# Kernel optimization log

Hardware: AMD Instinct MI355X
Metric: run time of the kernel (lower is better)

## Reference

```python
import math
import jax, jax.numpy as jnp
import numpy as np

L = 4        # n_layer
H = 8        # n_head
C = 512      # n_embd
V = 50257    # vocab_size
BLK = 1024   # block_size
R = 8        # lora_rank
LORA_SCALING = 32.0 / 8.0  # lora_alpha / lora_rank
B, T = 2, 1024


def _layernorm(x, g, b, eps=1e-5):
    m = jnp.mean(x, axis=-1, keepdims=True)
    v = jnp.var(x, axis=-1, keepdims=True)
    return (x - m) / jnp.sqrt(v + eps) * g + b


def _new_gelu(x):
    # 0.5*x*(1+tanh(sqrt(2/pi)*(x+0.044715*x^3)))
    return 0.5 * x * (1.0 + jnp.tanh(math.sqrt(2.0 / math.pi) * (x + 0.044715 * x ** 3)))


def _lora_linear(x, W, A, Bm):
    # nn.Linear (no bias) + LoRA low-rank update (dropout is identity in eval)
    return x @ W.T + LORA_SCALING * ((x @ A.T) @ Bm.T)


def setup_inputs() -> dict:
    key = jax.random.key(0)
    ks = jax.random.split(key, 16)
    s = 0.02  # GPT-2 init std
    inp = {
        'idx': jax.random.randint(ks[0], (B, T), 0, V, dtype=jnp.int64),
        'wte': jax.random.normal(ks[1], (V, C), jnp.float32) * s,
        'wpe': jax.random.normal(ks[2], (BLK, C), jnp.float32) * s,
        'ln1_g': jnp.ones((L, C), jnp.float32),
        'ln1_b': jnp.zeros((L, C), jnp.float32),
        'attn_w': jax.random.normal(ks[3], (L, 3 * C, C), jnp.float32) * s,
        'attn_lA': jax.random.normal(ks[4], (L, R, C), jnp.float32) * s,
        'attn_lB': jax.random.normal(ks[5], (L, 3 * C, R), jnp.float32) * s,
        'proj_w': jax.random.normal(ks[6], (L, C, C), jnp.float32) * (s / math.sqrt(2 * L)),
        'proj_lA': jax.random.normal(ks[7], (L, R, C), jnp.float32) * s,
        'proj_lB': jax.random.normal(ks[8], (L, C, R), jnp.float32) * s,
        'ln2_g': jnp.ones((L, C), jnp.float32),
        'ln2_b': jnp.zeros((L, C), jnp.float32),
        'fc_w': jax.random.normal(ks[9], (L, 4 * C, C), jnp.float32) * s,
        'fc_b': jnp.zeros((L, 4 * C), jnp.float32),
        'mproj_w': jax.random.normal(ks[10], (L, C, 4 * C), jnp.float32) * (s / math.sqrt(2 * L)),
        'mproj_b': jnp.zeros((L, C), jnp.float32),
        'lnf_g': jnp.ones((C,), jnp.float32),
        'lnf_b': jnp.zeros((C,), jnp.float32),
        'head_w': jax.random.normal(ks[11], (V, C), jnp.float32) * s,
    }
    return inp


def _gpt_forward(idx, wte, wpe, ln1_g, ln1_b, attn_w, attn_lA, attn_lB,
                 proj_w, proj_lA, proj_lB, ln2_g, ln2_b, fc_w, fc_b,
                 mproj_w, mproj_b, lnf_g, lnf_b, head_w):
    Bsz, Tlen = idx.shape
    hd = C // H
    x = wte[idx] + wpe[:Tlen][None, :, :]          # [B,T,C]
    mask = jnp.tril(jnp.ones((Tlen, Tlen), bool))  # causal mask
    for i in range(L):
        # --- attention ---
        h = _layernorm(x, ln1_g[i], ln1_b[i])
        qkv = _lora_linear(h, attn_w[i], attn_lA[i], attn_lB[i])  # [B,T,3C]
        q, k, v = jnp.split(qkv, 3, axis=-1)
        q = q.reshape(Bsz, Tlen, H, hd).transpose(0, 2, 1, 3)  # bhtd
        k = k.reshape(Bsz, Tlen, H, hd).transpose(0, 2, 1, 3)
        v = v.reshape(Bsz, Tlen, H, hd).transpose(0, 2, 1, 3)
        att = jnp.einsum('bhqd,bhkd->bhqk', q, k) * (1.0 / math.sqrt(hd))
        att = jnp.where(mask, att, -jnp.inf)
        att = jax.nn.softmax(att, axis=-1)
        y = jnp.einsum('bhqk,bhkd->bhqd', att, v)
        y = y.transpose(0, 2, 1, 3).reshape(Bsz, Tlen, C)
        y = _lora_linear(y, proj_w[i], proj_lA[i], proj_lB[i])
        x = x + y
        # --- MLP ---
        h2 = _layernorm(x, ln2_g[i], ln2_b[i])
        m = _new_gelu(h2 @ fc_w[i].T + fc_b[i]) @ mproj_w[i].T + mproj_b[i]
        x = x + m
    x = _layernorm(x, lnf_g, lnf_b)
    return x @ head_w.T  # logits [B,T,V]


def reference(idx, wte, wpe, ln1_g, ln1_b, attn_w, attn_lA, attn_lB,
              proj_w, proj_lA, proj_lB, ln2_g, ln2_b, fc_w, fc_b,
              mproj_w, mproj_b, lnf_g, lnf_b, head_w):
    return _gpt_forward(idx, wte, wpe, ln1_g, ln1_b, attn_w, attn_lA, attn_lB,
                        proj_w, proj_lA, proj_lB, ln2_g, ln2_b, fc_w, fc_b,
                        mproj_w, mproj_b, lnf_g, lnf_b, head_w)
```

## Files before the change

kernel.cpp:

```cpp
#include <hip/hip_runtime.h>
#include <cstdint>
#include <cstddef>

#define NLAYER 4
#define CDIM   512
#define TLEN   1024
#define BSZ    2
#define MROWS  (BSZ * TLEN)
#define VOCAB  50257
#define NHEAD  8
#define HDIM   64
#define LORA_S 4.0f

typedef unsigned short ushort_t;
typedef __attribute__((ext_vector_type(8))) short  short8;
typedef __attribute__((ext_vector_type(8))) _Float16 half8;
typedef __attribute__((ext_vector_type(4))) float  f32x4;
typedef __attribute__((ext_vector_type(4))) unsigned short us4;

__device__ inline ushort_t f2bf(float f) {
  union { float f; unsigned u; } c; c.f = f;
  unsigned u = c.u;
  u += 0x7fffu + ((u >> 16) & 1u);
  return (ushort_t)(u >> 16);
}

__device__ inline ushort_t f2h(float f) {
  union { _Float16 h; ushort_t u; } c; c.h = (_Float16)f;
  return c.u;
}

__device__ inline float gelu_f(float v) {
  float t = tanhf(0.7978845608028654f * (v + 0.044715f * v * v * v));
  return 0.5f * v * (1.0f + t);
}

__device__ inline void stage16(const ushort_t* g, ushort_t* lds) {
  __builtin_amdgcn_global_load_lds(
      (__attribute__((address_space(1))) unsigned int*)(g),
      (__attribute__((address_space(3))) unsigned int*)(lds),
      16, 0, 0);
}

template<int EPI>
__global__ __launch_bounds__(256) void gemm_bt(const ushort_t* __restrict__ A,
                                               const ushort_t* __restrict__ B,
                                               void* __restrict__ Cv,
                                               const float* __restrict__ bias,
                                               int M, int N, int K) {
  __shared__ ushort_t As[128 * 32];
  __shared__ ushort_t Bs[128 * 32];
  const int tid  = threadIdx.x;
  const int wave = tid >> 6, lane = tid & 63;
  const int m0 = blockIdx.y << 7;
  const int n0 = blockIdx.x << 7;
  const int wr = (wave >> 1) << 6;
  const int wc = (wave & 1) << 6;
  const int lr = lane & 15;
  const int kq = (lane >> 4) << 3;

  f32x4 acc[4][4];
#pragma unroll
  for (int i = 0; i < 4; ++i)
#pragma unroll
    for (int j = 0; j < 4; ++j) {
      acc[i][j][0] = 0.f; acc[i][j][1] = 0.f;
      acc[i][j][2] = 0.f; acc[i][j][3] = 0.f;
    }

  for (int k0 = 0; k0 < K; k0 += 32) {
    __syncthreads();
#pragma unroll
    for (int i = 0; i < 2; ++i) {
      int c = i * 256 + tid;
      int row = c >> 2, col = (c & 3) << 3;
      stage16(A + (size_t)(m0 + row) * K + k0 + col,
              As + ((i * 256 + (wave << 6)) << 3));
    }
#pragma unroll
    for (int i = 0; i < 2; ++i) {
      int c = i * 256 + tid;
      int row = c >> 2, col = (c & 3) << 3;
      int n = n0 + row; if (n > N - 1) n = N - 1;
      stage16(B + (size_t)n * K + k0 + col,
              Bs + ((i * 256 + (wave << 6)) << 3));
    }
    __syncthreads();

    short8 af[4], bf[4];
#pragma unroll
    for (int i = 0; i < 4; ++i)
      af[i] = *(const short8*)(As + (wr + i * 16 + lr) * 32 + kq);
#pragma unroll
    for (int j = 0; j < 4; ++j)
      bf[j] = *(const short8*)(Bs + (wc + j * 16 + lr) * 32 + kq);
#pragma unroll
    for (int i = 0; i < 4; ++i)
#pragma unroll
      for (int j = 0; j < 4; ++j)
        acc[i][j] = __builtin_amdgcn_mfma_f32_16x16x32_bf16(af[i], bf[j], acc[i][j], 0, 0, 0);
  }

  const int rq = (lane >> 4) << 2;
  const int cl = lane & 15;
#pragma unroll
  for (int i = 0; i < 4; ++i) {
    int mb = m0 + wr + i * 16 + rq;
#pragma unroll
    for (int j = 0; j < 4; ++j) {
      int col = n0 + wc + j * 16 + cl;
      if (col < N) {
        if (EPI == 0) {
          float* cp = (float*)Cv + (size_t)mb * N + col;
#pragma unroll
          for (int r = 0; r < 4; ++r) cp[(size_t)r * N] = acc[i][j][r];
        } else {
          ushort_t* cp = (ushort_t*)Cv + (size_t)mb * N + col;
          const float bb = bias[col];
#pragma unroll
          for (int r = 0; r < 4; ++r) cp[(size_t)r * N] = f2bf(gelu_f(acc[i][j][r] + bb));
        }
      }
    }
  }
}

__global__ __launch_bounds__(256) void gemm64_res(const ushort_t* __restrict__ A,
                                                  const ushort_t* __restrict__ B,
                                                  float* __restrict__ x,
                                                  const float* __restrict__ bias,
                                                  int M, int N, int K) {
  __shared__ ushort_t As[64 * 32];
  __shared__ ushort_t Bs[64 * 32];
  const int tid  = threadIdx.x;
  const int wave = tid >> 6, lane = tid & 63;
  const int m0 = blockIdx.y << 6;
  const int n0 = blockIdx.x << 6;
  const int wr = (wave >> 1) << 5;
  const int wc = (wave & 1) << 5;
  const int lr = lane & 15;
  const int kq = (lane >> 4) << 3;

  f32x4 acc[2][2];
#pragma unroll
  for (int i = 0; i < 2; ++i)
#pragma unroll
    for (int j = 0; j < 2; ++j) {
      acc[i][j][0] = 0.f; acc[i][j][1] = 0.f;
      acc[i][j][2] = 0.f; acc[i][j][3] = 0.f;
    }

  const int row = tid >> 2, col = (tid & 3) << 3;

  for (int k0 = 0; k0 < K; k0 += 32) {
    __syncthreads();
    stage16(A + (size_t)(m0 + row) * K + k0 + col, As + (wave << 9));
    stage16(B + (size_t)(n0 + row) * K + k0 + col, Bs + (wave << 9));
    __syncthreads();

    short8 af[2], bf[2];
#pragma unroll
    for (int i = 0; i < 2; ++i)
      af[i] = *(const short8*)(As + (wr + i * 16 + lr) * 32 + kq);
#pragma unroll
    for (int j = 0; j < 2; ++j)
      bf[j] = *(const short8*)(Bs + (wc + j * 16 + lr) * 32 + kq);
#pragma unroll
    for (int i = 0; i < 2; ++i)
#pragma unroll
      for (int j = 0; j < 2; ++j)
        acc[i][j] = __builtin_amdgcn_mfma_f32_16x16x32_bf16(af[i], bf[j], acc[i][j], 0, 0, 0);
  }

  const int rq = (lane >> 4) << 2;
  const int cl = lane & 15;
#pragma unroll
  for (int i = 0; i < 2; ++i) {
    int mb = m0 + wr + i * 16 + rq;
#pragma unroll
    for (int j = 0; j < 2; ++j) {
      int c = n0 + wc + j * 16 + cl;
      float bb = bias ? bias[c] : 0.f;
      float* xp = x + (size_t)mb * N + c;
#pragma unroll
      for (int r = 0; r < 4; ++r) xp[(size_t)r * N] = xp[(size_t)r * N] + acc[i][j][r] + bb;
    }
  }
}

__global__ void conv_bf16(const float* __restrict__ in, ushort_t* __restrict__ out, long n) {
  long i = ((long)blockIdx.x * 256 + threadIdx.x) * 4;
  if (i < n) {
    float4 v = *(const float4*)(in + i);
    us4 o = { f2bf(v.x), f2bf(v.y), f2bf(v.z), f2bf(v.w) };
    *(us4*)(out + i) = o;
  }
}

__global__ void conv_lora(const float* __restrict__ W, const float* __restrict__ lA,
                          const float* __restrict__ lB, ushort_t* __restrict__ out,
                          int N, long total) {
  long i = (long)blockIdx.x * 256 + threadIdx.x;
  if (i >= total) return;
  long nk = (long)N * CDIM;
  int  l  = (int)(i / nk);
  long r  = i - (long)l * nk;
  int  n  = (int)(r >> 9);
  int  k  = (int)(r & 511);
  const float* lAp = lA + (long)l * 8 * CDIM;
  const float* lBp = lB + (long)l * N * 8;
  float acc = W[i];
#pragma unroll
  for (int j = 0; j < 8; ++j) acc += LORA_S * lBp[n * 8 + j] * lAp[j * CDIM + k];
  out[i] = f2bf(acc);
}

__global__ void embed_kernel(const int* __restrict__ idx, const float* __restrict__ wte,
                             const float* __restrict__ wpe, float* __restrict__ x) {
  int i = blockIdx.x * 256 + threadIdx.x;
  int m = i >> 9, c = i & 511;
  int t = m & (TLEN - 1);
  x[i] = wte[(size_t)idx[m] * CDIM + c] + wpe[(size_t)t * CDIM + c];
}

__global__ __launch_bounds__(256) void ln_kernel(const float* __restrict__ x,
                                                 const float* __restrict__ g,
                                                 const float* __restrict__ b,
                                                 ushort_t* __restrict__ out) {
  const int m = blockIdx.x, tid = threadIdx.x;
  const float2 v = ((const float2*)(x + (size_t)m * CDIM))[tid];
  float s = v.x + v.y, ss = v.x * v.x + v.y * v.y;
#pragma unroll
  for (int off = 32; off; off >>= 1) { s += __shfl_xor(s, off); ss += __shfl_xor(ss, off); }
  __shared__ float rs[4], rss[4];
  const int w = tid >> 6, lane = tid & 63;
  if (lane == 0) { rs[w] = s; rss[w] = ss; }
  __syncthreads();
  s  = rs[0] + rs[1] + rs[2] + rs[3];
  ss = rss[0] + rss[1] + rss[2] + rss[3];
  const float mean = s * (1.f / CDIM);
  const float var  = ss * (1.f / CDIM) - mean * mean;
  const float rstd = rsqrtf(var + 1e-5f);
  const int c = tid * 2;
  out[(size_t)m * CDIM + c]     = f2bf((v.x - mean) * rstd * g[c]     + b[c]);
  out[(size_t)m * CDIM + c + 1] = f2bf((v.y - mean) * rstd * g[c + 1] + b[c + 1]);
}

__global__ __launch_bounds__(256) void attn_mfma(const float* __restrict__ qkv,
                                                 ushort_t* __restrict__ ybf) {
  __shared__ ushort_t Ks[32 * 72];
  __shared__ ushort_t Vt[64 * 40];
  __shared__ ushort_t Pl[4 * 16 * 40];

  const int tid  = threadIdx.x;
  const int wave = tid >> 6, lane = tid & 63;
  const int lr   = lane & 15;
  const int quad = lane >> 4;
  const int kq   = quad << 3;
  const int t0   = blockIdx.x << 6;
  const int bh   = blockIdx.y;
  const int bb   = bh >> 3, hh = bh & 7;
  const int qb   = t0 + (wave << 4);
  const size_t RS = 3 * CDIM;

  half8 aq[2];
  {
    const float* qr = qkv + (size_t)(bb * TLEN + qb + lr) * RS + hh * 64 + kq;
#pragma unroll
    for (int c = 0; c < 2; ++c) {
      float4 f0 = *(const float4*)(qr + c * 32);
      float4 f1 = *(const float4*)(qr + c * 32 + 4);
      half8 v;
      v[0] = (_Float16)f0.x; v[1] = (_Float16)f0.y;
      v[2] = (_Float16)f0.z; v[3] = (_Float16)f0.w;
      v[4] = (_Float16)f1.x; v[5] = (_Float16)f1.y;
      v[6] = (_Float16)f1.z; v[7] = (_Float16)f1.w;
      aq[c] = v;
    }
  }

  f32x4 o[4];
#pragma unroll
  for (int dt = 0; dt < 4; ++dt) { o[dt][0] = 0.f; o[dt][1] = 0.f; o[dt][2] = 0.f; o[dt][3] = 0.f; }
  float m[4] = { -1e30f, -1e30f, -1e30f, -1e30f };
  float l[4] = { 0.f, 0.f, 0.f, 0.f };

  const int kk    = tid & 31;
  const int dbase = (tid >> 5) << 3;

  const int ntiles = (blockIdx.x + 1) << 1;
  for (int kb = 0; kb < ntiles; ++kb) {
    const int kbase = kb << 5;
    __syncthreads();
    {
      const float* kp = qkv + (size_t)(bb * TLEN + kbase + kk) * RS + CDIM + hh * 64 + dbase;
      float4 f0 = *(const float4*)kp;
      float4 f1 = *(const float4*)(kp + 4);
      half8 kv;
      kv[0] = (_Float16)f0.x; kv[1] = (_Float16)f0.y;
      kv[2] = (_Float16)f0.z; kv[3] = (_Float16)f0.w;
      kv[4] = (_Float16)f1.x; kv[5] = (_Float16)f1.y;
      kv[6] = (_Float16)f1.z; kv[7] = (_Float16)f1.w;
      *(half8*)(Ks + kk * 72 + dbase) = kv;
      const float* vp = kp + CDIM;
      float4 g0 = *(const float4*)vp;
      float4 g1 = *(const float4*)(vp + 4);
      ushort_t vb[8] = { f2h(g0.x), f2h(g0.y), f2h(g0.z), f2h(g0.w),
                         f2h(g1.x), f2h(g1.y), f2h(g1.z), f2h(g1.w) };
#pragma unroll
      for (int j = 0; j < 8; ++j) Vt[(dbase + j) * 40 + kk] = vb[j];
    }
    __syncthreads();

    if (kbase <= qb + 15) {
      f32x4 st[2];
#pragma unroll
      for (int kt = 0; kt < 2; ++kt) {
        half8 b0 = *(const half8*)(Ks + (kt * 16 + lr) * 72 + kq);
        half8 b1 = *(const half8*)(Ks + (kt * 16 + lr) * 72 + 32 + kq);
        f32x4 acc = { 0.f, 0.f, 0.f, 0.f };
        acc = __builtin_amdgcn_mfma_f32_16x16x32_f16(aq[0], b0, acc, 0, 0, 0);
        acc = __builtin_amdgcn_mfma_f32_16x16x32_f16(aq[1], b1, acc, 0, 0, 0);
        st[kt] = acc;
      }
      float corr[4];
#pragma unroll
      for (int r = 0; r < 4; ++r) {
        const int qrow = qb + quad * 4 + r;
#pragma unroll
        for (int kt = 0; kt < 2; ++kt) {
          const int kcol = kbase + kt * 16 + lr;
          float s = st[kt][r] * 0.125f;
          st[kt][r] = (kcol <= qrow) ? s : -1e30f;
        }
        float mx = fmaxf(st[0][r], st[1][r]);
#pragma unroll
        for (int off = 8; off; off >>= 1) mx = fmaxf(mx, __shfl_xor(mx, off));
        const float mnew = fmaxf(m[r], mx);
        corr[r] = __expf(m[r] - mnew);
        m[r] = mnew;
        float p0 = __expf(st[0][r] - mnew);
        float p1 = __expf(st[1][r] - mnew);
        st[0][r] = p0; st[1][r] = p1;
        float ps = p0 + p1;
#pragma unroll
        for (int off = 8; off; off >>= 1) ps += __shfl_xor(ps, off);
        l[r] = l[r] * corr[r] + ps;
      }
#pragma unroll
      for (int dt = 0; dt < 4; ++dt)
#pragma unroll
        for (int r = 0; r < 4; ++r) o[dt][r] *= corr[r];
      ushort_t* pw = Pl + wave * 640;
#pragma unroll
      for (int kt = 0; kt < 2; ++kt)
#pragma unroll
        for (int r = 0; r < 4; ++r)
          pw[(quad * 4 + r) * 40 + kt * 16 + lr] = f2h(st[kt][r]);
      half8 ap = *(const half8*)(pw + lr * 40 + kq);
#pragma unroll
      for (int dt = 0; dt < 4; ++dt) {
        half8 bv = *(const half8*)(Vt + (dt * 16 + lr) * 40 + kq);
        o[dt] = __builtin_amdgcn_mfma_f32_16x16x32_f16(ap, bv, o[dt], 0, 0, 0);
      }
    }
  }

#pragma unroll
  for (int r = 0; r < 4; ++r) {
    const float inv = 1.0f / l[r];
    const int qrow = qb + quad * 4 + r;
    ushort_t* yp = ybf + (size_t)(bb * TLEN + qrow) * CDIM + hh * 64;
#pragma unroll
    for (int dt = 0; dt < 4; ++dt)
      yp[dt * 16 + lr] = f2bf(o[dt][r] * inv);
  }
}

extern "C" void kernel_launch(void* const* d_in, const int* in_sizes, int n_in,
                              void* d_out, int out_size, void* d_ws, size_t ws_size,
                              hipStream_t stream) {
  const int*   idx     = (const int*)  d_in[0];
  const float* wte     = (const float*)d_in[1];
  const float* wpe     = (const float*)d_in[2];
  const float* ln1_g   = (const float*)d_in[3];
  const float* ln1_b   = (const float*)d_in[4];
  const float* attn_w  = (const float*)d_in[5];
  const float* attn_lA = (const float*)d_in[6];
  const float* attn_lB = (const float*)d_in[7];
  const float* proj_w  = (const float*)d_in[8];
  const float* proj_lA = (const float*)d_in[9];
  const float* proj_lB = (const float*)d_in[10];
  const float* ln2_g   = (const float*)d_in[11];
  const float* ln2_b   = (const float*)d_in[12];
  const float* fc_w    = (const float*)d_in[13];
  const float* fc_b    = (const float*)d_in[14];
  const float* mproj_w = (const float*)d_in[15];
  const float* mproj_b = (const float*)d_in[16];
  const float* lnf_g   = (const float*)d_in[17];
  const float* lnf_b   = (const float*)d_in[18];
  const float* head_w  = (const float*)d_in[19];
  float* out = (float*)d_out;

  uintptr_t p = (uintptr_t)d_ws;
  auto take = [&](size_t bytes) -> void* {
    uintptr_t q = p;
    p = (p + bytes + 255) & ~(uintptr_t)255;
    return (void*)q;
  };
  ushort_t* wAttnB  = (ushort_t*)take((size_t)NLAYER * 1536 * 512 * 2);
  ushort_t* wProjB  = (ushort_t*)take((size_t)NLAYER * 512 * 512 * 2);
  ushort_t* wFcB    = (ushort_t*)take((size_t)NLAYER * 2048 * 512 * 2);
  ushort_t* wMprojB = (ushort_t*)take((size_t)NLAYER * 512 * 2048 * 2);
  ushort_t* wHeadB  = (ushort_t*)take((size_t)VOCAB * 512 * 2);
  float*    x       = (float*)   take((size_t)MROWS * 512 * 4);
  ushort_t* hbf     = (ushort_t*)take((size_t)MROWS * 512 * 2);
  float*    qkv     = (float*)   take((size_t)MROWS * 1536 * 4);
  ushort_t* ybf     = (ushort_t*)take((size_t)MROWS * 512 * 2);
  ushort_t* mbf     = (ushort_t*)take((size_t)MROWS * 2048 * 2);

  {
    long nA = (long)NLAYER * 1536 * 512;
    conv_lora<<<(int)((nA + 255) / 256), 256, 0, stream>>>(attn_w, attn_lA, attn_lB, wAttnB, 1536, nA);
    long nP = (long)NLAYER * 512 * 512;
    conv_lora<<<(int)((nP + 255) / 256), 256, 0, stream>>>(proj_w, proj_lA, proj_lB, wProjB, 512, nP);
    long nF = (long)NLAYER * 2048 * 512;
    conv_bf16<<<(int)((nF / 4 + 255) / 256), 256, 0, stream>>>(fc_w, wFcB, nF);
    long nM = (long)NLAYER * 512 * 2048;
    conv_bf16<<<(int)((nM / 4 + 255) / 256), 256, 0, stream>>>(mproj_w, wMprojB, nM);
    long nH = (long)VOCAB * 512;
    conv_bf16<<<(int)((nH / 4 + 255) / 256), 256, 0, stream>>>(head_w, wHeadB, nH);
  }

  embed_kernel<<<(MROWS * 512) / 256, 256, 0, stream>>>(idx, wte, wpe, x);

  for (int l = 0; l < NLAYER; ++l) {
    ln_kernel<<<MROWS, 256, 0, stream>>>(x, ln1_g + l * 512, ln1_b + l * 512, hbf);
    gemm_bt<0><<<dim3(1536 / 128, MROWS / 128), 256, 0, stream>>>(
        hbf, wAttnB + (size_t)l * 1536 * 512, qkv, nullptr, MROWS, 1536, 512);
    attn_mfma<<<dim3(TLEN / 64, BSZ * NHEAD), 256, 0, stream>>>(qkv, ybf);
    gemm64_res<<<dim3(512 / 64, MROWS / 64), 256, 0, stream>>>(
        ybf, wProjB + (size_t)l * 512 * 512, x, nullptr, MROWS, 512, 512);

    ln_kernel<<<MROWS, 256, 0, stream>>>(x, ln2_g + l * 512, ln2_b + l * 512, hbf);
    gemm_bt<2><<<dim3(2048 / 128, MROWS / 128), 256, 0, stream>>>(
        hbf, wFcB + (size_t)l * 2048 * 512, mbf, fc_b + l * 2048, MROWS, 2048, 512);
    gemm64_res<<<dim3(512 / 64, MROWS / 64), 256, 0, stream>>>(
        mbf, wMprojB + (size_t)l * 512 * 2048, x, mproj_b + l * 512, MROWS, 512, 2048);
  }

  ln_kernel<<<MROWS, 256, 0, stream>>>(x, lnf_g, lnf_b, hbf);
  gemm_bt<0><<<dim3((VOCAB + 127) / 128, MROWS / 128), 256, 0, stream>>>(
      hbf, wHeadB, out, nullptr, MROWS, VOCAB, 512);
}
```

Baseline: 1.337 ms.

## Swizzle GEMM workgroups across XCDs and fuse weight conversion launches

GEMM kernels now use a 1D grid and remap block ids so that each XCD gets a contiguous range of tiles, ordered m-fastest, to improve L2 reuse of weight tiles. The five weight-conversion launches are merged into two kernels that branch on the flat index. The embedding kernel is vectorised to float4. The cost is extra integer division per block and hardcoded grid sizes tied to the fixed shapes.

```diff
diff --git a/kernel.cpp b/kernel.cpp
--- a/kernel.cpp
+++ b/kernel.cpp
@@ -40,6 +40,12 @@
       (__attribute__((address_space(1))) unsigned int*)(g),
       (__attribute__((address_space(3))) unsigned int*)(lds),
       16, 0, 0);
+}
+
+__device__ inline int xcd_swz(int flat, int nwg) {
+  int q = nwg >> 3, r = nwg & 7;
+  int x = flat & 7, pos = flat >> 3;
+  return (x < r ? x * (q + 1) : r * (q + 1) + (x - r) * q) + pos;
 }
 
 template<int EPI>
@@ -52,8 +58,12 @@
   __shared__ ushort_t Bs[128 * 32];
   const int tid  = threadIdx.x;
   const int wave = tid >> 6, lane = tid & 63;
-  const int m0 = blockIdx.y << 7;
-  const int n0 = blockIdx.x << 7;
+  const int ntm  = M >> 7;
+  const int swz  = xcd_swz(blockIdx.x, gridDim.x);
+  const int nid  = swz / ntm;
+  const int mid  = swz - nid * ntm;
+  const int m0 = mid << 7;
+  const int n0 = nid << 7;
   const int wr = (wave >> 1) << 6;
   const int wc = (wave & 1) << 6;
   const int lr = lane & 15;
@@ -134,8 +144,12 @@
   __shared__ ushort_t Bs[64 * 32];
   const int tid  = threadIdx.x;
   const int wave = tid >> 6, lane = tid & 63;
-  const int m0 = blockIdx.y << 6;
-  const int n0 = blockIdx.x << 6;
+  const int ntm  = M >> 6;
+  const int swz  = xcd_swz(blockIdx.x, gridDim.x);
+  const int nid  = swz / ntm;
+  const int mid  = swz - nid * ntm;
+  const int m0 = mid << 6;
+  const int n0 = nid << 6;
   const int wr = (wave >> 1) << 5;
   const int wc = (wave & 1) << 5;
   const int lr = lane & 15;
@@ -188,39 +202,58 @@
   }
 }
 
-__global__ void conv_bf16(const float* __restrict__ in, ushort_t* __restrict__ out, long n) {
-  long i = ((long)blockIdx.x * 256 + threadIdx.x) * 4;
-  if (i < n) {
-    float4 v = *(const float4*)(in + i);
-    us4 o = { f2bf(v.x), f2bf(v.y), f2bf(v.z), f2bf(v.w) };
-    *(us4*)(out + i) = o;
-  }
-}
-
-__global__ void conv_lora(const float* __restrict__ W, const float* __restrict__ lA,
-                          const float* __restrict__ lB, ushort_t* __restrict__ out,
-                          int N, long total) {
+__global__ void conv_lora_all(const float* __restrict__ attn_w, const float* __restrict__ attn_lA,
+                              const float* __restrict__ attn_lB, const float* __restrict__ proj_w,
+                              const float* __restrict__ proj_lA, const float* __restrict__ proj_lB,
+                              ushort_t* __restrict__ wAttnB, ushort_t* __restrict__ wProjB) {
   long i = (long)blockIdx.x * 256 + threadIdx.x;
-  if (i >= total) return;
+  const long nA = (long)NLAYER * 1536 * CDIM;
+  const long nP = (long)NLAYER * 512 * CDIM;
+  const float* W; const float* lA; const float* lB; ushort_t* out; int N; long ii;
+  if (i < nA) { W = attn_w; lA = attn_lA; lB = attn_lB; out = wAttnB; N = 1536; ii = i; }
+  else {
+    ii = i - nA; if (ii >= nP) return;
+    W = proj_w; lA = proj_lA; lB = proj_lB; out = wProjB; N = 512;
+  }
   long nk = (long)N * CDIM;
-  int  l  = (int)(i / nk);
-  long r  = i - (long)l * nk;
+  int  l  = (int)(ii / nk);
+  long r  = ii - (long)l * nk;
   int  n  = (int)(r >> 9);
   int  k  = (int)(r & 511);
   const float* lAp = lA + (long)l * 8 * CDIM;
   const float* lBp = lB + (long)l * N * 8;
-  float acc = W[i];
+  float acc = W[ii];
 #pragma unroll
   for (int j = 0; j < 8; ++j) acc += LORA_S * lBp[n * 8 + j] * lAp[j * CDIM + k];
-  out[i] = f2bf(acc);
+  out[ii] = f2bf(acc);
+}
+
+__global__ void conv_bf16_all(const float* __restrict__ fc_w, const float* __restrict__ mproj_w,
+                              const float* __restrict__ head_w, ushort_t* __restrict__ wFcB,
+                              ushort_t* __restrict__ wMprojB, ushort_t* __restrict__ wHeadB) {
+  long j = ((long)blockIdx.x * 256 + threadIdx.x) * 4;
+  const long nF = (long)NLAYER * 2048 * CDIM;
+  const long nM = (long)NLAYER * CDIM * 2048;
+  const long nH = (long)VOCAB * CDIM;
+  const float* src; ushort_t* dst; long off;
+  if (j < nF)           { src = fc_w;    dst = wFcB;    off = j; }
+  else if (j < nF + nM) { src = mproj_w; dst = wMprojB; off = j - nF; }
+  else if (j < nF + nM + nH) { src = head_w; dst = wHeadB; off = j - nF - nM; }
+  else return;
+  float4 v = *(const float4*)(src + off);
+  us4 o = { f2bf(v.x), f2bf(v.y), f2bf(v.z), f2bf(v.w) };
+  *(us4*)(dst + off) = o;
 }
 
 __global__ void embed_kernel(const int* __restrict__ idx, const float* __restrict__ wte,
                              const float* __restrict__ wpe, float* __restrict__ x) {
-  int i = blockIdx.x * 256 + threadIdx.x;
+  int i = (blockIdx.x * 256 + threadIdx.x) * 4;
   int m = i >> 9, c = i & 511;
   int t = m & (TLEN - 1);
-  x[i] = wte[(size_t)idx[m] * CDIM + c] + wpe[(size_t)t * CDIM + c];
+  float4 a = *(const float4*)(wte + (size_t)idx[m] * CDIM + c);
+  float4 b = *(const float4*)(wpe + (size_t)t * CDIM + c);
+  float4 o = { a.x + b.x, a.y + b.y, a.z + b.z, a.w + b.w };
+  *(float4*)(x + i) = o;
 }
 
 __global__ __launch_bounds__(256) void ln_kernel(const float* __restrict__ x,
@@ -419,37 +452,28 @@
   ushort_t* ybf     = (ushort_t*)take((size_t)MROWS * 512 * 2);
   ushort_t* mbf     = (ushort_t*)take((size_t)MROWS * 2048 * 2);
 
-  {
-    long nA = (long)NLAYER * 1536 * 512;
-    conv_lora<<<(int)((nA + 255) / 256), 256, 0, stream>>>(attn_w, attn_lA, attn_lB, wAttnB, 1536, nA);
-    long nP = (long)NLAYER * 512 * 512;
-    conv_lora<<<(int)((nP + 255) / 256), 256, 0, stream>>>(proj_w, proj_lA, proj_lB, wProjB, 512, nP);
-    long nF = (long)NLAYER * 2048 * 512;
-    conv_bf16<<<(int)((nF / 4 + 255) / 256), 256, 0, stream>>>(fc_w, wFcB, nF);
-    long nM = (long)NLAYER * 512 * 2048;
-    conv_bf16<<<(int)((nM / 4 + 255) / 256), 256, 0, stream>>>(mproj_w, wMprojB, nM);
-    long nH = (long)VOCAB * 512;
-    conv_bf16<<<(int)((nH / 4 + 255) / 256), 256, 0, stream>>>(head_w, wHeadB, nH);
-  }
-
-  embed_kernel<<<(MROWS * 512) / 256, 256, 0, stream>>>(idx, wte, wpe, x);
+  conv_lora_all<<<16384, 256, 0, stream>>>(attn_w, attn_lA, attn_lB,
+                                           proj_w, proj_lA, proj_lB, wAttnB, wProjB);
+  conv_bf16_all<<<33321, 256, 0, stream>>>(fc_w, mproj_w, head_w, wFcB, wMprojB, wHeadB);
+
+  embed_kernel<<<(MROWS * 512 / 4) / 256, 256, 0, stream>>>(idx, wte, wpe, x);
 
   for (int l = 0; l < NLAYER; ++l) {
     ln_kernel<<<MROWS, 256, 0, stream>>>(x, ln1_g + l * 512, ln1_b + l * 512, hbf);
-    gemm_bt<0><<<dim3(1536 / 128, MROWS / 128), 256, 0, stream>>>(
+    gemm_bt<0><<<(1536 / 128) * (MROWS / 128), 256, 0, stream>>>(
         hbf, wAttnB + (size_t)l * 1536 * 512, qkv, nullptr, MROWS, 1536, 512);
     attn_mfma<<<dim3(TLEN / 64, BSZ * NHEAD), 256, 0, stream>>>(qkv, ybf);
-    gemm64_res<<<dim3(512 / 64, MROWS / 64), 256, 0, stream>>>(
+    gemm64_res<<<(512 / 64) * (MROWS / 64), 256, 0, stream>>>(
         ybf, wProjB + (size_t)l * 512 * 512, x, nullptr, MROWS, 512, 512);
 
     ln_kernel<<<MROWS, 256, 0, stream>>>(x, ln2_g + l * 512, ln2_b + l * 512, hbf);
-    gemm_bt<2><<<dim3(2048 / 128, MROWS / 128), 256, 0, stream>>>(
+    gemm_bt<2><<<(2048 / 128) * (MROWS / 128), 256, 0, stream>>>(
         hbf, wFcB + (size_t)l * 2048 * 512, mbf, fc_b + l * 2048, MROWS, 2048, 512);
-    gemm64_res<<<dim3(512 / 64, MROWS / 64), 256, 0, stream>>>(
+    gemm64_res<<<(512 / 64) * (MROWS / 64), 256, 0, stream>>>(
         mbf, wMprojB + (size_t)l * 512 * 2048, x, mproj_b + l * 512, MROWS, 512, 2048);
   }
 
   ln_kernel<<<MROWS, 256, 0, stream>>>(x, lnf_g, lnf_b, hbf);
-  gemm_bt<0><<<dim3((VOCAB + 127) / 128, MROWS / 128), 256, 0, stream>>>(
+  gemm_bt<0><<<((VOCAB + 127) / 128) * (MROWS / 128), 256, 0, stream>>>(
       hbf, wHeadB, out, nullptr, MROWS, VOCAB, 512);
 }
```

Measured after the change: 1.328 ms. About the same (-0.7%).
